# Kernel tuning notes

Hardware: AMD Instinct MI355X
Metric: run time of the kernel (lower is better)

The kernel has to match this reference:

```python
import jax, jax.numpy as jnp
import numpy as np

N = 50000
E = 800000
D_IN = 128
D_OUT = 64


def setup_inputs() -> dict:
    key = jax.random.key(0)
    ks = jax.random.split(key, 8)
    x = jax.random.normal(ks[0], (N, D_IN), dtype=jnp.float32)
    edge_index = jax.random.randint(ks[1], (2, E), 0, N, dtype=jnp.int64)
    s = 1.0 / np.sqrt(D_IN)
    # PyG SAGEConv: lin_l (applied to aggregated neighbors, has bias), lin_r (root, no bias)
    w1_l = jax.random.uniform(ks[2], (D_IN, D_IN), jnp.float32, -s, s)
    b1 = jnp.zeros((D_IN,), jnp.float32)
    w1_r = jax.random.uniform(ks[3], (D_IN, D_IN), jnp.float32, -s, s)
    w2_l = jax.random.uniform(ks[4], (D_IN, D_OUT), jnp.float32, -s, s)
    b2 = jnp.zeros((D_OUT,), jnp.float32)
    w2_r = jax.random.uniform(ks[5], (D_IN, D_OUT), jnp.float32, -s, s)
    return {"x": x, "edge_index": edge_index, "w1_l": w1_l, "b1": b1,
            "w1_r": w1_r, "w2_l": w2_l, "b2": b2, "w2_r": w2_r}


def _sage_conv(x, src, dst, w_l, b_l, w_r):
    # mean-aggregate source features at destination nodes
    msg_sum = jax.ops.segment_sum(x[src], dst, num_segments=N)  # [N, d]
    cnt = jax.ops.segment_sum(jnp.ones((src.shape[0],), x.dtype), dst, num_segments=N)
    mean = msg_sum / jnp.maximum(cnt, 1.0)[:, None]
    out = mean @ w_l + b_l + x @ w_r
    # L2 normalize (normalize=True)
    norm = jnp.linalg.norm(out, axis=-1, keepdims=True)
    return out / jnp.maximum(norm, 1e-12)


def reference(x, edge_index, w1_l, b1, w1_r, w2_l, b2, w2_r):
    src, dst = edge_index[0], edge_index[1]
    h = _sage_conv(x, src, dst, w1_l, b1, w1_r)
    h = _sage_conv(h, src, dst, w2_l, b2, w2_r)
    return h
```

## Files before the change

kernel.cpp:

```cpp
#include <hip/hip_runtime.h>
#include <math.h>

#define NN 50000
#define EE 800000
#define NB 196
#define CAP 6144

typedef __attribute__((ext_vector_type(8))) short bf16x8;
typedef __attribute__((ext_vector_type(16))) float f32x16;
typedef __attribute__((ext_vector_type(4))) unsigned short us4;

__device__ inline unsigned short bf16_rne(float f) {
    union { float f; unsigned u; } a; a.f = f;
    unsigned u = a.u;
    u += 0x7fff + ((u >> 16) & 1);
    return (unsigned short)(u >> 16);
}
__device__ inline float bf16_lo(unsigned v) {
    union { unsigned u; float f; } a; a.u = v << 16;
    return a.f;
}
__device__ inline float bf16_hi(unsigned v) {
    union { unsigned u; float f; } a; a.u = v & 0xffff0000u;
    return a.f;
}

__global__ void prep_all_kernel(const float* __restrict__ w1l, const float* __restrict__ w1r,
                                const float* __restrict__ w2l, const float* __restrict__ w2r,
                                unsigned short* __restrict__ wt1, unsigned short* __restrict__ wt2,
                                unsigned short* __restrict__ y1pad, unsigned short* __restrict__ y2pad,
                                int* __restrict__ bcur) {
    int idx = blockIdx.x * 256 + threadIdx.x;
    if (idx < 32768) {
        int n = idx >> 7, k = idx & 127;
        float v = (n < 128) ? w1l[(size_t)k * 128 + n] : w1r[(size_t)k * 128 + (n - 128)];
        wt1[idx] = bf16_rne(v);
    } else if (idx < 49152) {
        int j = idx - 32768;
        int n = j >> 7, k = j & 127;
        float v = (n < 64) ? w2l[(size_t)k * 64 + n] : w2r[(size_t)k * 64 + (n - 64)];
        wt2[j] = bf16_rne(v);
    } else {
        int j = idx - 49152;
        if (j < 128) y1pad[j] = 0;
        else if (j < 192) y2pad[j - 128] = 0;
        else if (j < 192 + NB) bcur[j - 192] = 0;
    }
}

__global__ __launch_bounds__(1024) void bin_kernel(
        const int* __restrict__ src, const int* __restrict__ dst,
        int* __restrict__ gcur, int* __restrict__ rec, int E) {
    __shared__ int hist[NB];
    __shared__ int cur[NB];
    const int t = threadIdx.x;
    const int per = (E + gridDim.x - 1) / gridDim.x;
    const int lo = blockIdx.x * per;
    const int hi = min(lo + per, E);

    for (int i = t; i < NB; i += 1024) hist[i] = 0;
    __syncthreads();
    for (int e = lo + t; e < hi; e += 1024)
        atomicAdd(&hist[dst[e] >> 8], 1);
    __syncthreads();
    for (int i = t; i < NB; i += 1024)
        cur[i] = atomicAdd(&gcur[i], hist[i]);
    __syncthreads();
    for (int e = lo + t; e < hi; e += 1024) {
        int d = dst[e], s = src[e];
        int cb = d >> 8;
        int p = atomicAdd(&cur[cb], 1);
        if (p < CAP) rec[(size_t)cb * CAP + p] = ((d & 255) << 16) | s;
    }
}

__global__ void scan2_kernel(const int* __restrict__ bcur, int* __restrict__ bsum, int nb) {
    __shared__ int s[256];
    int t = threadIdx.x;
    s[t] = (t < nb) ? bcur[t] : 0;
    __syncthreads();
    for (int ofs = 1; ofs < 256; ofs <<= 1) {
        int v = s[t];
        int a = (t >= ofs) ? s[t - ofs] : 0;
        __syncthreads();
        s[t] = v + a;
        __syncthreads();
    }
    if (t < nb) bsum[t] = (t == 0) ? 0 : s[t - 1];
}

__global__ __launch_bounds__(256) void place_kernel(
        const int* __restrict__ rec, const int* __restrict__ bcur,
        const int* __restrict__ bsum, int* __restrict__ rowoff,
        unsigned short* __restrict__ csr, int n) {
    __shared__ int cnt[256];
    __shared__ int cur[256];
    __shared__ unsigned short sorted[CAP];
    const int cb = blockIdx.x, t = threadIdx.x;
    int m = bcur[cb]; if (m > CAP) m = CAP;
    const int* r = rec + (size_t)cb * CAP;
    const int base = bsum[cb];

    cnt[t] = 0;
    __syncthreads();
    for (int i = t; i < m; i += 256) atomicAdd(&cnt[r[i] >> 16], 1);
    __syncthreads();
    int orig = cnt[t];
    for (int ofs = 1; ofs < 256; ofs <<= 1) {
        int v = cnt[t];
        int a = (t >= ofs) ? cnt[t - ofs] : 0;
        __syncthreads();
        cnt[t] = v + a;
        __syncthreads();
    }
    int excl = cnt[t] - orig;
    int node = cb * 256 + t;
    if (node < n) rowoff[node] = base + excl;
    if (node == n - 1) rowoff[n] = base + cnt[t];
    cur[t] = excl;
    __syncthreads();
    for (int i = t; i < m; i += 256) {
        int rr = r[i];
        int pos = atomicAdd(&cur[rr >> 16], 1);
        sorted[pos] = (unsigned short)(rr & 0xffff);
    }
    __syncthreads();
    for (int i = t; i < m; i += 256) csr[base + i] = sorted[i];
}

template <int CO, bool BF16IN>
__global__ __launch_bounds__(256) void transform_mfma_kernel(
        const void* __restrict__ xin, const unsigned short* __restrict__ wt,
        const float* __restrict__ bias, unsigned short* __restrict__ ybuf,
        float* __restrict__ rbuf, int n) {
    constexpr int HALF = CO / 2;
    constexpr int LDW = 136;
    __shared__ unsigned short Xs[64][LDW];
    __shared__ unsigned short Ws[64][LDW];

    const int t = threadIdx.x;
    const int node0 = blockIdx.x * 64;
    const int gy = blockIdx.y;

    if (BF16IN) {
        const unsigned short* xb = (const unsigned short*)xin;
        for (int e = t; e < 64 * 16; e += 256) {
            int nd = e >> 4, c8 = e & 15;
            int node = node0 + nd;
            int4 v = (node < n) ? ((const int4*)(xb + (size_t)node * 128))[c8]
                                : make_int4(0, 0, 0, 0);
            *(int4*)&Xs[nd][c8 * 8] = v;
        }
    } else {
        const float* xf = (const float*)xin;
        for (int e = t; e < 64 * 32; e += 256) {
            int nd = e >> 5, c4 = e & 31;
            int node = node0 + nd;
            float4 v = (node < n) ? ((const float4*)xf)[(size_t)node * 32 + c4]
                                  : make_float4(0.f, 0.f, 0.f, 0.f);
            us4 p;
            p.x = bf16_rne(v.x); p.y = bf16_rne(v.y); p.z = bf16_rne(v.z); p.w = bf16_rne(v.w);
            *(us4*)&Xs[nd][c4 * 4] = p;
        }
    }
    for (int e = t; e < 64 * 16; e += 256) {
        int nd = e >> 4, c8 = e & 15;
        int4 v = ((const int4*)(wt + ((size_t)(gy * 64 + nd)) * 128))[c8];
        *(int4*)&Ws[nd][c8 * 8] = v;
    }
    __syncthreads();

    const int lane = t & 63, wave = t >> 6;
    const int wm = (wave & 1) * 32, wn = (wave >> 1) * 32;
    const int ml = wm + (lane & 31);
    const int nl = wn + (lane & 31);
    const int koff = (lane >> 5) * 8;

    f32x16 acc;
#pragma unroll
    for (int r = 0; r < 16; r++) acc[r] = 0.f;

#pragma unroll
    for (int kk = 0; kk < 8; kk++) {
        bf16x8 a = *(const bf16x8*)&Xs[ml][kk * 16 + koff];
        bf16x8 b = *(const bf16x8*)&Ws[nl][kk * 16 + koff];
        acc = __builtin_amdgcn_mfma_f32_32x32x16_bf16(a, b, acc, 0, 0, 0);
    }

    const int col = gy * 64 + wn + (lane & 31);
    if (col < HALF) {
#pragma unroll
        for (int r = 0; r < 16; r++) {
            int row = (r & 3) + 8 * (r >> 2) + 4 * (lane >> 5);
            int node = node0 + wm + row;
            if (node < n) ybuf[(size_t)node * HALF + col] = bf16_rne(acc[r]);
        }
    } else {
        const float bj = bias[col - HALF];
#pragma unroll
        for (int r = 0; r < 16; r++) {
            int row = (r & 3) + 8 * (r >> 2) + 4 * (lane >> 5);
            int node = node0 + wm + row;
            if (node < n) rbuf[(size_t)node * HALF + (col - HALF)] = acc[r] + bj;
        }
    }
}

template <bool OUTBF16>
__global__ __launch_bounds__(256) void gather128_kernel(
        const unsigned short* __restrict__ y, const float* __restrict__ rr,
        const int* __restrict__ rowoff, const unsigned short* __restrict__ csr,
        void* __restrict__ out, int n) {
    const int wave = threadIdx.x >> 6;
    const int lane = threadIdx.x & 63;
    const int node = blockIdx.x * 4 + wave;
    if (node >= n) return;

    const int off = rowoff[node];
    const int end = rowoff[node + 1];
    const int deg = end - off;

    float2 acc = make_float2(0.f, 0.f);
    for (int k0 = 0; k0 < deg; k0 += 16) {
        int idx[16];
#pragma unroll
        for (int i = 0; i < 16; i++) {
            int kk = off + k0 + i;
            idx[i] = (kk < end) ? (int)csr[kk] : n;
        }
        unsigned v[16];
#pragma unroll
        for (int i = 0; i < 16; i++)
            v[i] = *(const unsigned*)(y + (size_t)idx[i] * 128 + 2 * lane);
#pragma unroll
        for (int i = 0; i < 16; i++) {
            acc.x += bf16_lo(v[i]);
            acc.y += bf16_hi(v[i]);
        }
    }
    float im = 1.0f / fmaxf((float)deg, 1.0f);
    float2 rv = *(const float2*)(rr + (size_t)node * 128 + 2 * lane);
    float2 v = make_float2(acc.x * im + rv.x, acc.y * im + rv.y);
    float s = v.x * v.x + v.y * v.y;
#pragma unroll
    for (int m = 32; m >= 1; m >>= 1) s += __shfl_xor(s, m, 64);
    float rn = 1.0f / fmaxf(sqrtf(s), 1e-12f);
    v.x *= rn; v.y *= rn;
    if (OUTBF16) {
        unsigned pk = (unsigned)bf16_rne(v.x) | ((unsigned)bf16_rne(v.y) << 16);
        *(unsigned*)((unsigned short*)out + (size_t)node * 128 + 2 * lane) = pk;
    } else {
        *(float2*)((float*)out + (size_t)node * 128 + 2 * lane) = v;
    }
}

__global__ __launch_bounds__(256) void gather64_kernel(
        const unsigned short* __restrict__ y, const float* __restrict__ rr,
        const int* __restrict__ rowoff, const unsigned short* __restrict__ csr,
        float* __restrict__ out, int n) {
    const int wave = threadIdx.x >> 6;
    const int lane = threadIdx.x & 63;
    const int node = blockIdx.x * 4 + wave;
    if (node >= n) return;
    const int half = lane >> 5;
    const int l32 = lane & 31;

    const int off = rowoff[node];
    const int end = rowoff[node + 1];
    const int deg = end - off;
    const int P = (deg + 1) >> 1;

    float2 acc = make_float2(0.f, 0.f);
    for (int p0 = 0; p0 < P; p0 += 8) {
        int idx[8];
#pragma unroll
        for (int i = 0; i < 8; i++) {
            int kk = off + 2 * (p0 + i) + half;
            idx[i] = (kk < end) ? (int)csr[kk] : n;
        }
        unsigned v[8];
#pragma unroll
        for (int i = 0; i < 8; i++)
            v[i] = *(const unsigned*)(y + (size_t)idx[i] * 64 + 2 * l32);
#pragma unroll
        for (int i = 0; i < 8; i++) {
            acc.x += bf16_lo(v[i]);
            acc.y += bf16_hi(v[i]);
        }
    }
    acc.x += __shfl_xor(acc.x, 32, 64);
    acc.y += __shfl_xor(acc.y, 32, 64);

    float im = 1.0f / fmaxf((float)deg, 1.0f);
    float2 rv = *(const float2*)(rr + (size_t)node * 64 + 2 * l32);
    float2 v = make_float2(acc.x * im + rv.x, acc.y * im + rv.y);
    float s = v.x * v.x + v.y * v.y;
#pragma unroll
    for (int m = 32; m >= 1; m >>= 1) s += __shfl_xor(s, m, 64);
    s *= 0.5f;
    float rn = 1.0f / fmaxf(sqrtf(s), 1e-12f);
    if (half == 0)
        *(float2*)(out + (size_t)node * 64 + 2 * l32) = make_float2(v.x * rn, v.y * rn);
}

extern "C" void kernel_launch(void* const* d_in, const int* in_sizes, int n_in,
                              void* d_out, int out_size, void* d_ws, size_t ws_size,
                              hipStream_t stream) {
    const float* x   = (const float*)d_in[0];
    const int*   ei  = (const int*)d_in[1];
    const float* w1l = (const float*)d_in[2];
    const float* b1  = (const float*)d_in[3];
    const float* w1r = (const float*)d_in[4];
    const float* w2l = (const float*)d_in[5];
    const float* b2  = (const float*)d_in[6];
    const float* w2r = (const float*)d_in[7];
    float* out = (float*)d_out;

    const int* src = ei;
    const int* dst = ei + EE;

    char* ws = (char*)d_ws;
    auto align = [](size_t v) { return (v + 255) & ~(size_t)255; };
    int*   rowoff = (int*)ws;                 size_t o = align((size_t)(NN + 1) * 4);
    int*   bcur   = (int*)(ws + o);           o += align((size_t)NB * 4);
    int*   bsum   = (int*)(ws + o);           o += align((size_t)NB * 4);
    int*   rec    = (int*)(ws + o);           o += align((size_t)NB * CAP * 4);
    unsigned short* csr = (unsigned short*)(ws + o); o += align((size_t)EE * 2);
    unsigned short* wt1 = (unsigned short*)(ws + o); o += align((size_t)256 * 128 * 2);
    unsigned short* wt2 = (unsigned short*)(ws + o); o += align((size_t)128 * 128 * 2);
    unsigned short* y1  = (unsigned short*)(ws + o); o += align((size_t)(NN + 1) * 128 * 2);
    float*          r1  = (float*)(ws + o);          o += align((size_t)NN * 128 * 4);
    unsigned short* h1  = (unsigned short*)(ws + o); o += align((size_t)NN * 128 * 2);
    unsigned short* y2  = (unsigned short*)(ws + o); o += align((size_t)(NN + 1) * 64 * 2);
    float*          r2  = (float*)(ws + o);          o += align((size_t)NN * 64 * 4);

    prep_all_kernel<<<194, 256, 0, stream>>>(w1l, w1r, w2l, w2r, wt1, wt2,
                                             y1 + (size_t)NN * 128, y2 + (size_t)NN * 64, bcur);
    bin_kernel<<<128, 1024, 0, stream>>>(src, dst, bcur, rec, EE);
    scan2_kernel<<<1, 256, 0, stream>>>(bcur, bsum, NB);
    place_kernel<<<NB, 256, 0, stream>>>(rec, bcur, bsum, rowoff, csr, NN);

    transform_mfma_kernel<256, false><<<dim3((NN + 63) / 64, 4), 256, 0, stream>>>(
        x, wt1, b1, y1, r1, NN);
    gather128_kernel<true><<<(NN + 3) / 4, 256, 0, stream>>>(y1, r1, rowoff, csr, h1, NN);

    transform_mfma_kernel<128, true><<<dim3((NN + 63) / 64, 2), 256, 0, stream>>>(
        h1, wt2, b2, y2, r2, NN);
    gather64_kernel<<<(NN + 3) / 4, 256, 0, stream>>>(y2, r2, rowoff, csr, out, NN);
}
```

Before: 205.5 us.

## Vectorize gathers with 16-byte loads, store root term in bf16, fold scan into place

The gather kernels now split each wave into lane groups that each fetch a 16-byte chunk of a neighbor row. Several neighbors are processed in parallel, and the partial sums are combined with cross-lane shuffles. This replaces the per-lane 4-byte loads and is meant to reduce the number of memory transactions. The root/bias term is now stored as bf16 instead of fp32, which halves its traffic at some cost in precision. The standalone bucket scan kernel is merged into place_kernel, with each block recomputing the scan redundantly, which saves one launch. bin_kernel is also launched with twice as many blocks.

```diff
diff --git a/kernel.cpp b/kernel.cpp
--- a/kernel.cpp
+++ b/kernel.cpp
@@ -74,32 +74,28 @@
     }
 }
 
-__global__ void scan2_kernel(const int* __restrict__ bcur, int* __restrict__ bsum, int nb) {
-    __shared__ int s[256];
-    int t = threadIdx.x;
-    s[t] = (t < nb) ? bcur[t] : 0;
-    __syncthreads();
-    for (int ofs = 1; ofs < 256; ofs <<= 1) {
-        int v = s[t];
-        int a = (t >= ofs) ? s[t - ofs] : 0;
-        __syncthreads();
-        s[t] = v + a;
-        __syncthreads();
-    }
-    if (t < nb) bsum[t] = (t == 0) ? 0 : s[t - 1];
-}
-
 __global__ __launch_bounds__(256) void place_kernel(
         const int* __restrict__ rec, const int* __restrict__ bcur,
-        const int* __restrict__ bsum, int* __restrict__ rowoff,
-        unsigned short* __restrict__ csr, int n) {
+        int* __restrict__ rowoff, unsigned short* __restrict__ csr, int n) {
+    __shared__ int bscan[256];
     __shared__ int cnt[256];
     __shared__ int cur[256];
     __shared__ unsigned short sorted[CAP];
     const int cb = blockIdx.x, t = threadIdx.x;
+
+    bscan[t] = (t < NB) ? bcur[t] : 0;
+    __syncthreads();
+    for (int ofs = 1; ofs < 256; ofs <<= 1) {
+        int v = bscan[t];
+        int a = (t >= ofs) ? bscan[t - ofs] : 0;
+        __syncthreads();
+        bscan[t] = v + a;
+        __syncthreads();
+    }
+    const int base = (cb == 0) ? 0 : bscan[cb - 1];
+
     int m = bcur[cb]; if (m > CAP) m = CAP;
     const int* r = rec + (size_t)cb * CAP;
-    const int base = bsum[cb];
 
     cnt[t] = 0;
     __syncthreads();
@@ -132,7 +128,7 @@
 __global__ __launch_bounds__(256) void transform_mfma_kernel(
         const void* __restrict__ xin, const unsigned short* __restrict__ wt,
         const float* __restrict__ bias, unsigned short* __restrict__ ybuf,
-        float* __restrict__ rbuf, int n) {
+        unsigned short* __restrict__ rbuf, int n) {
     constexpr int HALF = CO / 2;
     constexpr int LDW = 136;
     __shared__ unsigned short Xs[64][LDW];
@@ -201,106 +197,137 @@
         for (int r = 0; r < 16; r++) {
             int row = (r & 3) + 8 * (r >> 2) + 4 * (lane >> 5);
             int node = node0 + wm + row;
-            if (node < n) rbuf[(size_t)node * HALF + (col - HALF)] = acc[r] + bj;
-        }
-    }
-}
-
-template <bool OUTBF16>
+            if (node < n) rbuf[(size_t)node * HALF + (col - HALF)] = bf16_rne(acc[r] + bj);
+        }
+    }
+}
+
 __global__ __launch_bounds__(256) void gather128_kernel(
-        const unsigned short* __restrict__ y, const float* __restrict__ rr,
+        const unsigned short* __restrict__ y, const unsigned short* __restrict__ rrb,
         const int* __restrict__ rowoff, const unsigned short* __restrict__ csr,
-        void* __restrict__ out, int n) {
+        unsigned short* __restrict__ out, int n) {
     const int wave = threadIdx.x >> 6;
     const int lane = threadIdx.x & 63;
     const int node = blockIdx.x * 4 + wave;
     if (node >= n) return;
+    const int g = lane >> 4;
+    const int q = lane & 15;
 
     const int off = rowoff[node];
     const int end = rowoff[node + 1];
     const int deg = end - off;
 
-    float2 acc = make_float2(0.f, 0.f);
-    for (int k0 = 0; k0 < deg; k0 += 16) {
-        int idx[16];
-#pragma unroll
-        for (int i = 0; i < 16; i++) {
-            int kk = off + k0 + i;
-            idx[i] = (kk < end) ? (int)csr[kk] : n;
-        }
-        unsigned v[16];
-#pragma unroll
-        for (int i = 0; i < 16; i++)
-            v[i] = *(const unsigned*)(y + (size_t)idx[i] * 128 + 2 * lane);
-#pragma unroll
-        for (int i = 0; i < 16; i++) {
-            acc.x += bf16_lo(v[i]);
-            acc.y += bf16_hi(v[i]);
-        }
-    }
-    float im = 1.0f / fmaxf((float)deg, 1.0f);
-    float2 rv = *(const float2*)(rr + (size_t)node * 128 + 2 * lane);
-    float2 v = make_float2(acc.x * im + rv.x, acc.y * im + rv.y);
-    float s = v.x * v.x + v.y * v.y;
-#pragma unroll
-    for (int m = 32; m >= 1; m >>= 1) s += __shfl_xor(s, m, 64);
-    float rn = 1.0f / fmaxf(sqrtf(s), 1e-12f);
-    v.x *= rn; v.y *= rn;
-    if (OUTBF16) {
-        unsigned pk = (unsigned)bf16_rne(v.x) | ((unsigned)bf16_rne(v.y) << 16);
-        *(unsigned*)((unsigned short*)out + (size_t)node * 128 + 2 * lane) = pk;
-    } else {
-        *(float2*)((float*)out + (size_t)node * 128 + 2 * lane) = v;
+    float acc[8];
+#pragma unroll
+    for (int j = 0; j < 8; j++) acc[j] = 0.f;
+
+    for (int k0 = 0; k0 < deg; k0 += 8) {
+        int kk0 = off + k0 + g;
+        int kk1 = off + k0 + 4 + g;
+        int i0 = (kk0 < end) ? (int)csr[kk0] : n;
+        int i1 = (kk1 < end) ? (int)csr[kk1] : n;
+        uint4 v0 = *(const uint4*)(y + (size_t)i0 * 128 + q * 8);
+        uint4 v1 = *(const uint4*)(y + (size_t)i1 * 128 + q * 8);
+        const unsigned* u0 = (const unsigned*)&v0;
+        const unsigned* u1 = (const unsigned*)&v1;
+#pragma unroll
+        for (int i = 0; i < 4; i++) {
+            acc[2 * i]     += bf16_lo(u0[i]) + bf16_lo(u1[i]);
+            acc[2 * i + 1] += bf16_hi(u0[i]) + bf16_hi(u1[i]);
+        }
+    }
+#pragma unroll
+    for (int j = 0; j < 8; j++) {
+        acc[j] += __shfl_xor(acc[j], 16, 64);
+        acc[j] += __shfl_xor(acc[j], 32, 64);
+    }
+    const float im = 1.0f / fmaxf((float)deg, 1.0f);
+    uint4 rv = *(const uint4*)(rrb + (size_t)node * 128 + q * 8);
+    const unsigned* ru = (const unsigned*)&rv;
+    float v[8];
+    float ss = 0.f;
+#pragma unroll
+    for (int i = 0; i < 4; i++) {
+        v[2 * i]     = acc[2 * i] * im     + bf16_lo(ru[i]);
+        v[2 * i + 1] = acc[2 * i + 1] * im + bf16_hi(ru[i]);
+    }
+#pragma unroll
+    for (int j = 0; j < 8; j++) ss += v[j] * v[j];
+#pragma unroll
+    for (int m = 8; m >= 1; m >>= 1) ss += __shfl_xor(ss, m, 64);
+    const float rn = 1.0f / fmaxf(sqrtf(ss), 1e-12f);
+    if (g == 0) {
+        uint4 pk;
+        unsigned* pu = (unsigned*)&pk;
+#pragma unroll
+        for (int i = 0; i < 4; i++)
+            pu[i] = (unsigned)bf16_rne(v[2 * i] * rn) |
+                    ((unsigned)bf16_rne(v[2 * i + 1] * rn) << 16);
+        *(uint4*)(out + (size_t)node * 128 + q * 8) = pk;
     }
 }
 
 __global__ __launch_bounds__(256) void gather64_kernel(
-        const unsigned short* __restrict__ y, const float* __restrict__ rr,
+        const unsigned short* __restrict__ y, const unsigned short* __restrict__ rrb,
         const int* __restrict__ rowoff, const unsigned short* __restrict__ csr,
         float* __restrict__ out, int n) {
     const int wave = threadIdx.x >> 6;
     const int lane = threadIdx.x & 63;
     const int node = blockIdx.x * 4 + wave;
     if (node >= n) return;
-    const int half = lane >> 5;
-    const int l32 = lane & 31;
+    const int g = lane >> 3;
+    const int q = lane & 7;
 
     const int off = rowoff[node];
     const int end = rowoff[node + 1];
     const int deg = end - off;
-    const int P = (deg + 1) >> 1;
-
-    float2 acc = make_float2(0.f, 0.f);
-    for (int p0 = 0; p0 < P; p0 += 8) {
-        int idx[8];
-#pragma unroll
-        for (int i = 0; i < 8; i++) {
-            int kk = off + 2 * (p0 + i) + half;
-            idx[i] = (kk < end) ? (int)csr[kk] : n;
-        }
-        unsigned v[8];
-#pragma unroll
-        for (int i = 0; i < 8; i++)
-            v[i] = *(const unsigned*)(y + (size_t)idx[i] * 64 + 2 * l32);
-#pragma unroll
-        for (int i = 0; i < 8; i++) {
-            acc.x += bf16_lo(v[i]);
-            acc.y += bf16_hi(v[i]);
-        }
-    }
-    acc.x += __shfl_xor(acc.x, 32, 64);
-    acc.y += __shfl_xor(acc.y, 32, 64);
-
-    float im = 1.0f / fmaxf((float)deg, 1.0f);
-    float2 rv = *(const float2*)(rr + (size_t)node * 64 + 2 * l32);
-    float2 v = make_float2(acc.x * im + rv.x, acc.y * im + rv.y);
-    float s = v.x * v.x + v.y * v.y;
-#pragma unroll
-    for (int m = 32; m >= 1; m >>= 1) s += __shfl_xor(s, m, 64);
-    s *= 0.5f;
-    float rn = 1.0f / fmaxf(sqrtf(s), 1e-12f);
-    if (half == 0)
-        *(float2*)(out + (size_t)node * 64 + 2 * l32) = make_float2(v.x * rn, v.y * rn);
+
+    float acc[8];
+#pragma unroll
+    for (int j = 0; j < 8; j++) acc[j] = 0.f;
+
+    for (int k0 = 0; k0 < deg; k0 += 16) {
+        int kk0 = off + k0 + g;
+        int kk1 = off + k0 + 8 + g;
+        int i0 = (kk0 < end) ? (int)csr[kk0] : n;
+        int i1 = (kk1 < end) ? (int)csr[kk1] : n;
+        uint4 v0 = *(const uint4*)(y + (size_t)i0 * 64 + q * 8);
+        uint4 v1 = *(const uint4*)(y + (size_t)i1 * 64 + q * 8);
+        const unsigned* u0 = (const unsigned*)&v0;
+        const unsigned* u1 = (const unsigned*)&v1;
+#pragma unroll
+        for (int i = 0; i < 4; i++) {
+            acc[2 * i]     += bf16_lo(u0[i]) + bf16_lo(u1[i]);
+            acc[2 * i + 1] += bf16_hi(u0[i]) + bf16_hi(u1[i]);
+        }
+    }
+#pragma unroll
+    for (int j = 0; j < 8; j++) {
+        acc[j] += __shfl_xor(acc[j], 8, 64);
+        acc[j] += __shfl_xor(acc[j], 16, 64);
+        acc[j] += __shfl_xor(acc[j], 32, 64);
+    }
+    const float im = 1.0f / fmaxf((float)deg, 1.0f);
+    uint4 rv = *(const uint4*)(rrb + (size_t)node * 64 + q * 8);
+    const unsigned* ru = (const unsigned*)&rv;
+    float v[8];
+    float ss = 0.f;
+#pragma unroll
+    for (int i = 0; i < 4; i++) {
+        v[2 * i]     = acc[2 * i] * im     + bf16_lo(ru[i]);
+        v[2 * i + 1] = acc[2 * i + 1] * im + bf16_hi(ru[i]);
+    }
+#pragma unroll
+    for (int j = 0; j < 8; j++) ss += v[j] * v[j];
+#pragma unroll
+    for (int m = 4; m >= 1; m >>= 1) ss += __shfl_xor(ss, m, 64);
+    const float rn = 1.0f / fmaxf(sqrtf(ss), 1e-12f);
+    if (g == 0) {
+        float4 o0 = make_float4(v[0] * rn, v[1] * rn, v[2] * rn, v[3] * rn);
+        float4 o1 = make_float4(v[4] * rn, v[5] * rn, v[6] * rn, v[7] * rn);
+        *(float4*)(out + (size_t)node * 64 + q * 8) = o0;
+        *(float4*)(out + (size_t)node * 64 + q * 8 + 4) = o1;
+    }
 }
 
 extern "C" void kernel_launch(void* const* d_in, const int* in_sizes, int n_in,
@@ -323,26 +350,24 @@
     auto align = [](size_t v) { return (v + 255) & ~(size_t)255; };
     int*   rowoff = (int*)ws;                 size_t o = align((size_t)(NN + 1) * 4);
     int*   bcur   = (int*)(ws + o);           o += align((size_t)NB * 4);
-    int*   bsum   = (int*)(ws + o);           o += align((size_t)NB * 4);
     int*   rec    = (int*)(ws + o);           o += align((size_t)NB * CAP * 4);
     unsigned short* csr = (unsigned short*)(ws + o); o += align((size_t)EE * 2);
     unsigned short* wt1 = (unsigned short*)(ws + o); o += align((size_t)256 * 128 * 2);
     unsigned short* wt2 = (unsigned short*)(ws + o); o += align((size_t)128 * 128 * 2);
     unsigned short* y1  = (unsigned short*)(ws + o); o += align((size_t)(NN + 1) * 128 * 2);
-    float*          r1  = (float*)(ws + o);          o += align((size_t)NN * 128 * 4);
+    unsigned short* r1  = (unsigned short*)(ws + o); o += align((size_t)NN * 128 * 2);
     unsigned short* h1  = (unsigned short*)(ws + o); o += align((size_t)NN * 128 * 2);
     unsigned short* y2  = (unsigned short*)(ws + o); o += align((size_t)(NN + 1) * 64 * 2);
-    float*          r2  = (float*)(ws + o);          o += align((size_t)NN * 64 * 4);
+    unsigned short* r2  = (unsigned short*)(ws + o); o += align((size_t)NN * 64 * 2);
 
     prep_all_kernel<<<194, 256, 0, stream>>>(w1l, w1r, w2l, w2r, wt1, wt2,
                                              y1 + (size_t)NN * 128, y2 + (size_t)NN * 64, bcur);
-    bin_kernel<<<128, 1024, 0, stream>>>(src, dst, bcur, rec, EE);
-    scan2_kernel<<<1, 256, 0, stream>>>(bcur, bsum, NB);
-    place_kernel<<<NB, 256, 0, stream>>>(rec, bcur, bsum, rowoff, csr, NN);
+    bin_kernel<<<256, 1024, 0, stream>>>(src, dst, bcur, rec, EE);
+    place_kernel<<<NB, 256, 0, stream>>>(rec, bcur, rowoff, csr, NN);
 
     transform_mfma_kernel<256, false><<<dim3((NN + 63) / 64, 4), 256, 0, stream>>>(
         x, wt1, b1, y1, r1, NN);
-    gather128_kernel<true><<<(NN + 3) / 4, 256, 0, stream>>>(y1, r1, rowoff, csr, h1, NN);
+    gather128_kernel<<<(NN + 3) / 4, 256, 0, stream>>>(y1, r1, rowoff, csr, h1, NN);
 
     transform_mfma_kernel<128, true><<<dim3((NN + 63) / 64, 2), 256, 0, stream>>>(
         h1, wt2, b2, y2, r2, NN);
```

Result: faster. 201.2 us (-2.1%).
